# Kernel tuning notes

Measured on AMD Instinct MI355X. Metric: run time of the kernel, lower is better.

## Reference

```python
import jax, jax.numpy as jnp
import numpy as np

HEADS, HD = 8, 64

def swish(x):
    return x * jax.nn.sigmoid(x)

def layer_norm(x, eps=1e-5):
    mu = jnp.mean(x, axis=-1, keepdims=True)
    var = jnp.var(x, axis=-1, keepdims=True)
    return (x - mu) / jnp.sqrt(var + eps)

def setup_inputs() -> dict:
    key = jax.random.key(0)
    k1, k2, k3 = jax.random.split(key, 3)
    B, L, D = 2, 2048, 512
    x = jax.random.normal(k1, (B, L, D), jnp.float32)
    cnn_w = jax.random.normal(k2, (HEADS * HD * 3, D, 3), jnp.float32) * 0.02
    cnn_b = jnp.zeros((HEADS * HD * 3,), jnp.float32)
    fc_w = jax.random.normal(k3, (D, HEADS * HD), jnp.float32) * 0.02
    fc_b = jnp.zeros((D,), jnp.float32)
    return {"x": x, "cnn_w": cnn_w, "cnn_b": cnn_b, "fc_w": fc_w, "fc_b": fc_b}

def reference(x, cnn_w, cnn_b, fc_w, fc_b):
    B, L, D = x.shape
    # Conv1d(dims -> heads*hd*3, kernel=3, stride=1, pad=1) on channel-first layout
    xt = jnp.transpose(x, (0, 2, 1))  # [B, D, L]
    y = jax.lax.conv_general_dilated(
        xt, cnn_w, window_strides=(1,), padding=[(1, 1)],
        dimension_numbers=("NCH", "OIH", "NCH"),
    ) + cnn_b[None, :, None]  # [B, 3*H*HD, L]
    qkv = swish(y).reshape(B, HEADS, HD * 3, L)
    q, k, v = jnp.split(qkv, 3, axis=-2)  # each [B, H, HD, L]
    # NOTE: original scales by sqrt(length), not sqrt(hd)
    scores = jnp.einsum("bhdw,bhdm->bhwm", q, k) / jnp.sqrt(jnp.float32(L))
    att = jax.nn.softmax(scores, axis=-1)  # [B, H, L, L]
    new_v = jnp.einsum("bhwm,bhdm->bwhd", att, v).reshape(B, L, HEADS * HD)
    m = swish(new_v @ fc_w.T + fc_b)  # [B, L, D]
    return layer_norm(x * 2 + m)
```

## Files before the change

kernel.cpp:

```cpp
#include <hip/hip_runtime.h>
#include <hip/hip_bf16.h>

#define BB 2
#define LL 2048
#define DD 512
#define HH 8
#define HDM 64
#define SCALE 0.022097086912079608f
#define QSCALE 0.03187935766f

typedef __hip_bfloat16 bf16;
typedef unsigned short u16;
typedef __attribute__((ext_vector_type(8))) short short8v;
typedef __attribute__((ext_vector_type(4))) float float4v;

#define XN  2097152
#define WN  2359296
#define BN  1536
#define FWN 262144
#define FBN 512

__device__ __forceinline__ float b2f(u16 u) {
    return __uint_as_float(((unsigned int)u) << 16);
}
__device__ __forceinline__ u16 f2u(float f) {
    bf16 h = __float2bfloat16(f);
    u16 r;
    __builtin_memcpy(&r, &h, 2);
    return r;
}
__device__ __forceinline__ uint4 pack8(const float* f) {
    uint4 p;
    p.x = (unsigned)f2u(f[0]) | ((unsigned)f2u(f[1]) << 16);
    p.y = (unsigned)f2u(f[2]) | ((unsigned)f2u(f[3]) << 16);
    p.z = (unsigned)f2u(f[4]) | ((unsigned)f2u(f[5]) << 16);
    p.w = (unsigned)f2u(f[6]) | ((unsigned)f2u(f[7]) << 16);
    return p;
}

__device__ __forceinline__ void gld_lds16(const u16* g, u16* l) {
    __builtin_amdgcn_global_load_lds(
        (const __attribute__((address_space(1))) unsigned int*)g,
        (__attribute__((address_space(3))) unsigned int*)l, 16, 0, 0);
}

__device__ __forceinline__ int detect_flag(const u16* __restrict__ xraw) {
    int bad = 0;
    int lane = threadIdx.x & 63;
    for (int i = lane; i < 256; i += 64) {
        float v = b2f(xraw[i]);
        if (!(fabsf(v) < 100.f)) bad = 1;
    }
    return (__ballot(bad) != 0ull) ? 1 : 0;
}

__device__ __forceinline__ void conv8(const void* src, u16* dst, size_t i, int flag) {
    if (flag) {
        const float* s = (const float*)src;
        float f[8];
        float4 a = *(const float4*)(s + i);
        float4 b = *(const float4*)(s + i + 4);
        f[0] = a.x; f[1] = a.y; f[2] = a.z; f[3] = a.w;
        f[4] = b.x; f[5] = b.y; f[6] = b.z; f[7] = b.w;
        *(uint4*)(dst + i) = pack8(f);
    } else {
        *(uint4*)(dst + i) = *(const uint4*)((const u16*)src + i);
    }
}

__global__ __launch_bounds__(256) void prep_kernel(
    const void* __restrict__ xsrc, const void* __restrict__ wsrc,
    const void* __restrict__ bsrc, const void* __restrict__ fwsrc,
    const void* __restrict__ fbsrc,
    u16* __restrict__ xp, u16* __restrict__ wt,
    u16* __restrict__ bc, u16* __restrict__ fwc, u16* __restrict__ fbc)
{
    const int flag = detect_flag((const u16*)xsrc);
    const int bid = blockIdx.x;

    if (bid < 1024) {
        int idx = bid * 256 + threadIdx.x;
        if (idx < 256) {
            int b2  = idx >> 7;
            int r2  = (idx >> 6) & 1;
            int c82 = (idx & 63) * 8;
            size_t off = ((size_t)(b2 * 2050 + (r2 ? 2049 : 0))) * 512 + c82;
            uint4 z = {0u, 0u, 0u, 0u};
            *(uint4*)(xp + off) = z;
        }
        int b   = idx / (LL * 64);
        int rem = idx - b * (LL * 64);
        int l   = rem >> 6;
        int c8  = (rem & 63) * 8;
        size_t si = ((size_t)(b * LL + l)) * 512 + c8;
        size_t di = ((size_t)(b * 2050 + l + 1)) * 512 + c8;
        if (flag) {
            const float* s = (const float*)xsrc;
            float f[8];
            float4 a = *(const float4*)(s + si);
            float4 bq = *(const float4*)(s + si + 4);
            f[0] = a.x; f[1] = a.y; f[2] = a.z; f[3] = a.w;
            f[4] = bq.x; f[5] = bq.y; f[6] = bq.z; f[7] = bq.w;
            *(uint4*)(xp + di) = pack8(f);
        } else {
            *(uint4*)(xp + di) = *(const uint4*)((const u16*)xsrc + si);
        }
    } else if (bid < 2176) {
        int idx = (bid - 1024) * 256 + threadIdx.x;
        int i8  = idx & 63;
        int rem = idx >> 6;
        int k   = rem % 3;
        int o   = rem / 3;
        float f[8];
        if (flag) {
            const float* s = (const float*)wsrc;
#pragma unroll
            for (int j = 0; j < 8; ++j) f[j] = s[(size_t)o * 1536 + (i8 * 8 + j) * 3 + k];
        } else {
            const u16* s = (const u16*)wsrc;
#pragma unroll
            for (int j = 0; j < 8; ++j) f[j] = b2f(s[(size_t)o * 1536 + (i8 * 8 + j) * 3 + k]);
        }
        *(uint4*)(wt + (size_t)o * 1536 + k * 512 + i8 * 8) = pack8(f);
    } else {
        int o = (bid - 2176) * 256 + threadIdx.x;
        if (o < BN / 8) {
            conv8(bsrc, bc, (size_t)o * 8, flag);
        } else if (o < BN / 8 + FWN / 8) {
            conv8(fwsrc, fwc, (size_t)(o - BN / 8) * 8, flag);
        } else if (o < BN / 8 + FWN / 8 + FBN / 8) {
            conv8(fbsrc, fbc, (size_t)(o - BN / 8 - FWN / 8) * 8, flag);
        }
    }
}

__global__ __launch_bounds__(256) void conv_mfma_kernel(
    const u16* __restrict__ xp,
    const u16* __restrict__ wt,
    const u16* __restrict__ bias,
    u16* __restrict__ qkbuf,
    u16* __restrict__ vbuf)
{
    __shared__ u16 smem[32768];
    u16* Asb = smem;
    u16* Bsb = smem + 2 * 128 * 64;
#define OTS 140
    u16* OT  = smem;

    const int blk = blockIdx.x;
    const int rt = blk / 12;
    const int ct = blk - rt * 12;
    const int b  = rt >> 4;
    const int l0 = (rt & 15) * 128;
    const int tid  = threadIdx.x;
    const int wave = tid >> 6;
    const int lane = tid & 63;
    const int quad = lane >> 4;
    const int l16  = lane & 15;
    const int e7   = l16 & 7;
    const int wx = wave & 1;
    const int wy = wave >> 1;

    float4v acc[4][4];
#pragma unroll
    for (int mt = 0; mt < 4; ++mt)
#pragma unroll
        for (int nt = 0; nt < 4; ++nt) acc[mt][nt] = (float4v){0.f, 0.f, 0.f, 0.f};

    const int rowW = wave * 32;
    const int lrow = lane >> 3;
    const int g8   = (((lane & 7) ^ lrow)) * 8;
    auto stage = [&](int kc, int buf) {
        const int slab = kc >> 3;
        const int i0   = (kc & 7) * 64;
        const u16* ga = xp + ((size_t)(b * 2050 + l0 + rowW + slab + lrow)) * 512 + i0 + g8;
        const u16* gb = wt + ((size_t)(ct * 128 + rowW + lrow)) * 1536 + kc * 64 + g8;
        u16* la = Asb + (size_t)(buf * 128 + rowW) * 64;
        u16* lb = Bsb + (size_t)(buf * 128 + rowW) * 64;
#pragma unroll
        for (int j = 0; j < 4; ++j) {
            gld_lds16(ga + (size_t)(j * 8) * 512,  la + (j * 8) * 64);
            gld_lds16(gb + (size_t)(j * 8) * 1536, lb + (j * 8) * 64);
        }
    };

    stage(0, 0);

    for (int kc = 0; kc < 24; ++kc) {
        const int cur = kc & 1;
        __syncthreads();

        if (kc < 23) stage(kc + 1, 1 - cur);

#pragma unroll
        for (int half = 0; half < 2; ++half) {
            const int p = ((half * 4 + quad) ^ e7) * 8;
            short8v aF[4], bF[4];
#pragma unroll
            for (int mt = 0; mt < 4; ++mt)
                aF[mt] = *(const short8v*)&Asb[(size_t)(cur * 128 + wy * 64 + mt * 16 + l16) * 64 + p];
#pragma unroll
            for (int nt = 0; nt < 4; ++nt)
                bF[nt] = *(const short8v*)&Bsb[(size_t)(cur * 128 + wx * 64 + nt * 16 + l16) * 64 + p];
#pragma unroll
            for (int mt = 0; mt < 4; ++mt)
#pragma unroll
                for (int nt = 0; nt < 4; ++nt)
                    acc[mt][nt] = __builtin_amdgcn_mfma_f32_16x16x32_bf16(
                        aF[mt], bF[nt], acc[mt][nt], 0, 0, 0);
        }
    }

    __syncthreads();
    {
        const int tloc = (ct * 2 + wx) % 3;
#pragma unroll
        for (int nt = 0; nt < 4; ++nt) {
            int oc = wx * 64 + nt * 16 + l16;
            float bb = b2f(bias[ct * 128 + oc]);
#pragma unroll
            for (int mt = 0; mt < 4; ++mt)
#pragma unroll
                for (int r = 0; r < 4; ++r) {
                    int lr = wy * 64 + mt * 16 + quad * 4 + r;
                    float y = acc[mt][nt][r] + bb;
                    y = y / (1.f + __expf(-y));
                    if (tloc == 0) y *= QSCALE;
                    OT[lr * OTS + oc] = f2u(y);
                }
        }
    }
    __syncthreads();

#pragma unroll
    for (int g = 0; g < 2; ++g) {
        int a  = ct * 2 + g;
        int t  = a % 3;
        int bh = b * HH + a / 3;
        if (t != 2) {
            u16* base = qkbuf + ((size_t)((bh * 2 + t) * LL + l0)) * HDM;
#pragma unroll
            for (int it = 0; it < 4; ++it) {
                int idx = it * 256 + tid;
                int l   = idx >> 3;
                int d8  = (idx & 7) * 8;
                uint4 val = *(const uint4*)&OT[l * OTS + g * 64 + d8];
                *(uint4*)(base + (size_t)l * HDM + d8) = val;
            }
        } else {
            u16* base = vbuf + ((size_t)(bh * HDM)) * LL + l0;
#pragma unroll
            for (int it = 0; it < 4; ++it) {
                int idx = it * 256 + tid;
                int dd  = idx >> 4;
                int p   = idx & 15;
                int l8  = p * 8;
                u16 tmp[8];
#pragma unroll
                for (int j = 0; j < 8; ++j) tmp[j] = OT[(l8 + j) * OTS + g * 64 + dd];
                int a32 = p >> 2;
                int pb_ = p & 3;
                int q2  = (2 * pb_) & 3;
                int h2  = pb_ >> 1;
                int n0  = 32 * a32 + 8 * q2 + 4 * h2;
                uint2 v0, v1;
                v0.x = (unsigned)tmp[0] | ((unsigned)tmp[1] << 16);
                v0.y = (unsigned)tmp[2] | ((unsigned)tmp[3] << 16);
                v1.x = (unsigned)tmp[4] | ((unsigned)tmp[5] << 16);
                v1.y = (unsigned)tmp[6] | ((unsigned)tmp[7] << 16);
                *(uint2*)(base + (size_t)dd * LL + n0)     = v0;
                *(uint2*)(base + (size_t)dd * LL + n0 + 8) = v1;
            }
        }
    }
#undef OTS
}

__global__ __launch_bounds__(512) void attn_mfma_kernel(
    const u16* __restrict__ qk,
    const u16* __restrict__ v,
    u16* __restrict__ newv)
{
    __shared__ u16 smem[32768];
    u16 (*kts)[2][64][64] = (u16 (*)[2][64][64])smem;
    u16 (*vts)[2][64][64] = (u16 (*)[2][64][64])(smem + 16384);

    const int lb = ((blockIdx.x & 7) << 5) + (blockIdx.x >> 3);
    const int bh = lb >> 4;
    const int qc = lb & 15;
    const int b  = bh >> 3;
    const int h  = bh & 7;
    const int tid  = threadIdx.x;
    const int wave = tid >> 6;
    const int kg   = wave >> 2;
    const int qg   = wave & 3;
    const int lane = tid & 63;
    const int quad = lane >> 4;
    const int l16  = lane & 15;
    const int e7   = l16 & 7;

    const u16* qbase = qk + ((size_t)(bh * 2 + 0)) * LL * HDM;
    const u16* kbase = qk + ((size_t)(bh * 2 + 1)) * LL * HDM;
    const u16* vbase = v + (size_t)bh * HDM * LL;

    const int q0 = qc * 128 + qg * 32;

    short8v qfrag[2][2];
#pragma unroll
    for (int sg = 0; sg < 2; ++sg) {
        const u16* qr = qbase + (size_t)(q0 + sg * 16 + l16) * HDM + quad * 8;
        qfrag[sg][0] = *(const short8v*)(qr);
        qfrag[sg][1] = *(const short8v*)(qr + 32);
    }

    short8v vones;
    {
        short o1 = (l16 == 0) ? (short)0x3F80 : (short)0;
#pragma unroll
        for (int j = 0; j < 8; ++j) vones[j] = o1;
    }

    float4v oacc[2][4];
    float4v lacc[2];
#pragma unroll
    for (int sg = 0; sg < 2; ++sg) {
        lacc[sg] = (float4v){0.f, 0.f, 0.f, 0.f};
#pragma unroll
        for (int dt = 0; dt < 4; ++dt) oacc[sg][dt] = (float4v){0.f, 0.f, 0.f, 0.f};
    }

    const int rr  = qg * 8 + (lane >> 3);
    const int sw8 = ((lane & 7) ^ (lane >> 3)) * 8;
    auto stage = [&](int ic, int buf) {
        const int m0 = ic * 64;
#pragma unroll
        for (int r = 0; r < 2; ++r) {
            gld_lds16(kbase + (size_t)(m0 + r * 32 + rr) * HDM + sw8,
                      &kts[kg][buf][r * 32 + qg * 8][0]);
            gld_lds16(vbase + (size_t)(r * 32 + rr) * LL + m0 + sw8,
                      &vts[kg][buf][r * 32 + qg * 8][0]);
        }
    };

    stage(kg, 0);

    for (int i = 0; i < 16; ++i) {
        const int cur = i & 1;
        __syncthreads();

        if (i < 15) stage(2 * (i + 1) + kg, 1 - cur);

        float4v s[2][4];
#pragma unroll
        for (int mt = 0; mt < 4; ++mt) {
            short8v b0 = *(const short8v*)&kts[kg][cur][mt * 16 + l16][((quad) ^ e7) * 8];
            short8v b1 = *(const short8v*)&kts[kg][cur][mt * 16 + l16][((quad + 4) ^ e7) * 8];
#pragma unroll
            for (int sg = 0; sg < 2; ++sg) {
                float4v t = (float4v){0.f, 0.f, 0.f, 0.f};
                t = __builtin_amdgcn_mfma_f32_16x16x32_bf16(b0, qfrag[sg][0], t, 0, 0, 0);
                t = __builtin_amdgcn_mfma_f32_16x16x32_bf16(b1, qfrag[sg][1], t, 0, 0, 0);
                s[sg][mt] = t;
            }
        }

        unsigned pk[2][4][2];
#pragma unroll
        for (int sg = 0; sg < 2; ++sg)
#pragma unroll
            for (int mt = 0; mt < 4; ++mt) {
                float p0 = __builtin_amdgcn_exp2f(s[sg][mt][0]);
                float p1 = __builtin_amdgcn_exp2f(s[sg][mt][1]);
                float p2 = __builtin_amdgcn_exp2f(s[sg][mt][2]);
                float p3 = __builtin_amdgcn_exp2f(s[sg][mt][3]);
                pk[sg][mt][0] = (unsigned)f2u(p0) | ((unsigned)f2u(p1) << 16);
                pk[sg][mt][1] = (unsigned)f2u(p2) | ((unsigned)f2u(p3) << 16);
            }

#pragma unroll
        for (int mu = 0; mu < 2; ++mu) {
            short8v pb[2];
#pragma unroll
            for (int sg = 0; sg < 2; ++sg) {
                union { short8v v8; unsigned u[4]; } U;
                U.u[0] = pk[sg][2 * mu][0];
                U.u[1] = pk[sg][2 * mu][1];
                U.u[2] = pk[sg][2 * mu + 1][0];
                U.u[3] = pk[sg][2 * mu + 1][1];
                pb[sg] = U.v8;
                lacc[sg] = __builtin_amdgcn_mfma_f32_16x16x32_bf16(vones, pb[sg], lacc[sg], 0, 0, 0);
            }
#pragma unroll
            for (int dt = 0; dt < 4; ++dt) {
                short8v va = *(const short8v*)&vts[kg][cur][dt * 16 + l16][((mu * 4 + quad) ^ e7) * 8];
#pragma unroll
                for (int sg = 0; sg < 2; ++sg)
                    oacc[sg][dt] = __builtin_amdgcn_mfma_f32_16x16x32_bf16(va, pb[sg], oacc[sg][dt], 0, 0, 0);
            }
        }
    }

    float dnm[2];
#pragma unroll
    for (int sg = 0; sg < 2; ++sg) dnm[sg] = __shfl(lacc[sg][0], l16);

    __syncthreads();
    float* xch = (float*)smem;
    if (kg == 1) {
#pragma unroll
        for (int sg = 0; sg < 2; ++sg) {
#pragma unroll
            for (int dt = 0; dt < 4; ++dt)
#pragma unroll
                for (int r = 0; r < 4; ++r)
                    xch[((qg * 34 + (sg * 16 + dt * 4 + r)) << 6) + lane] = oacc[sg][dt][r];
            xch[((qg * 34 + 32 + sg) << 6) + lane] = dnm[sg];
        }
    }
    __syncthreads();
    if (kg == 0) {
        u16* ob = newv + (size_t)b * LL * 512 + h * 64;
#pragma unroll
        for (int sg = 0; sg < 2; ++sg) {
            float dt2 = dnm[sg] + xch[((qg * 34 + 32 + sg) << 6) + lane];
            float inv = 1.f / dt2;
            const size_t orow = (size_t)(q0 + sg * 16 + l16) * 512 + quad * 4;
#pragma unroll
            for (int dt = 0; dt < 4; ++dt) {
                float o0 = oacc[sg][dt][0] + xch[((qg * 34 + (sg * 16 + dt * 4 + 0)) << 6) + lane];
                float o1 = oacc[sg][dt][1] + xch[((qg * 34 + (sg * 16 + dt * 4 + 1)) << 6) + lane];
                float o2 = oacc[sg][dt][2] + xch[((qg * 34 + (sg * 16 + dt * 4 + 2)) << 6) + lane];
                float o3 = oacc[sg][dt][3] + xch[((qg * 34 + (sg * 16 + dt * 4 + 3)) << 6) + lane];
                unsigned lo = (unsigned)f2u(o0 * inv) | ((unsigned)f2u(o1 * inv) << 16);
                unsigned hi = (unsigned)f2u(o2 * inv) | ((unsigned)f2u(o3 * inv) << 16);
                uint2 val; val.x = lo; val.y = hi;
                *(uint2*)(ob + orow + dt * 16) = val;
            }
        }
    }
}

__global__ __launch_bounds__(256) void fc_ln_mfma_kernel(
    const u16* __restrict__ newv,
    const u16* __restrict__ fcw,
    const u16* __restrict__ fcb,
    const u16* __restrict__ xp,
    const u16* __restrict__ xraw,
    void* __restrict__ out)
{
    const int flag = detect_flag(xraw);
    const int l0 = blockIdx.x * 16;
    const int tid  = threadIdx.x;
    const int wave = tid >> 6;
    const int lane = tid & 63;
    const int quad = lane >> 4;
    const int l16  = lane & 15;
    const int col0 = wave * 128;

    const int bb_ = l0 >> 11;
    const size_t xbase = ((size_t)(bb_ * 2050 + (l0 & 2047) + 1)) * 512;

    __shared__ float psum[4][16], psq[4][16];

    short8v aF[16];
    const u16* arow = newv + (size_t)(l0 + l16) * 512 + quad * 8;
#pragma unroll
    for (int kc = 0; kc < 16; ++kc)
        aF[kc] = *(const short8v*)(arow + kc * 32);

    float4v acc[8];
#pragma unroll
    for (int nt = 0; nt < 8; ++nt) acc[nt] = (float4v){0.f, 0.f, 0.f, 0.f};

#pragma unroll
    for (int nt = 0; nt < 8; ++nt) {
        const u16* brow = fcw + (size_t)(col0 + nt * 16 + l16) * 512 + quad * 8;
#pragma unroll
        for (int kc = 0; kc < 16; ++kc) {
            short8v bF = *(const short8v*)(brow + kc * 32);
            acc[nt] = __builtin_amdgcn_mfma_f32_16x16x32_bf16(aF[kc], bF, acc[nt], 0, 0, 0);
        }
    }

    float z[8][4];
    float rs[4] = {0.f, 0.f, 0.f, 0.f}, rq[4] = {0.f, 0.f, 0.f, 0.f};
#pragma unroll
    for (int nt = 0; nt < 8; ++nt) {
        int col = col0 + nt * 16 + l16;
        float bb = b2f(fcb[col]);
#pragma unroll
        for (int r = 0; r < 4; ++r) {
            int row = quad * 4 + r;
            float y = acc[nt][r] + bb;
            float sw = y / (1.f + __expf(-y));
            float xv = b2f(xp[xbase + (size_t)row * 512 + col]);
            float zz = xv * 2.f + sw;
            z[nt][r] = zz;
            rs[r] += zz;
            rq[r] += zz * zz;
        }
    }
#pragma unroll
    for (int msk = 1; msk <= 8; msk <<= 1)
#pragma unroll
        for (int r = 0; r < 4; ++r) {
            rs[r] += __shfl_xor(rs[r], msk);
            rq[r] += __shfl_xor(rq[r], msk);
        }
    if (l16 == 0) {
#pragma unroll
        for (int r = 0; r < 4; ++r) {
            psum[wave][quad * 4 + r] = rs[r];
            psq[wave][quad * 4 + r]  = rq[r];
        }
    }
    __syncthreads();

    float mu[4], inv[4];
#pragma unroll
    for (int r = 0; r < 4; ++r) {
        int row = quad * 4 + r;
        float s = psum[0][row] + psum[1][row] + psum[2][row] + psum[3][row];
        float q = psq[0][row] + psq[1][row] + psq[2][row] + psq[3][row];
        float m = s * (1.f / 512.f);
        float var = q * (1.f / 512.f) - m * m;
        mu[r] = m;
        inv[r] = rsqrtf(var + 1e-5f);
    }

#pragma unroll
    for (int nt = 0; nt < 8; ++nt) {
        int col = col0 + nt * 16 + l16;
#pragma unroll
        for (int r = 0; r < 4; ++r) {
            int row = quad * 4 + r;
            float val = (z[nt][r] - mu[r]) * inv[r];
            if (flag) ((float*)out)[(size_t)(l0 + row) * 512 + col] = val;
            else      ((u16*)out)[(size_t)(l0 + row) * 512 + col] = f2u(val);
        }
    }
}

extern "C" void kernel_launch(void* const* d_in, const int* in_sizes, int n_in,
                              void* d_out, int out_size, void* d_ws, size_t ws_size,
                              hipStream_t stream) {
    (void)in_sizes; (void)n_in; (void)out_size; (void)ws_size;

    char* ws = (char*)d_ws;
    u16* xp   = (u16*)(ws + 256);
    u16* wtc  = (u16*)(ws + 4198656);
    u16* bc   = (u16*)(ws + 8917248);
    u16* fwc  = (u16*)(ws + 8920320);
    u16* fbc  = (u16*)(ws + 9444608);
    u16* qkb  = (u16*)(ws + 9445632);
    u16* vb   = (u16*)(ws + 17834240);
    u16* nvc  = (u16*)(ws + 22028544);

    prep_kernel<<<dim3(2305), dim3(256), 0, stream>>>(
        d_in[0], d_in[1], d_in[2], d_in[3], d_in[4],
        xp, wtc, bc, fwc, fbc);

    conv_mfma_kernel<<<dim3(32 * 12), dim3(256), 0, stream>>>(xp, wtc, bc, qkb, vb);
    attn_mfma_kernel<<<dim3(256), dim3(512), 0, stream>>>(qkb, vb, nvc);
    fc_ln_mfma_kernel<<<dim3(256), dim3(256), 0, stream>>>(
        nvc, fwc, fbc, xp, (const u16*)d_in[0], d_out);
}
```

Before: 154.9 us.

## Stage conv weight transpose through LDS and widen FC+LayerNorm block to 8 waves

The conv-weight repacking in the prep kernel now has each block load 8 output rows with coalesced vector loads into shared memory and do the (i,k)->(k,i) transpose there. Previously each thread made strided scalar global reads. The FC+LayerNorm kernel moves to 512 threads, each wave covering 64 output columns instead of 128. It stages the A tile in LDS via gld_lds16 with an XOR swizzle to cut redundant global loads and per-wave register pressure. The costs are extra LDS use, a barrier, and shared-memory reads with 3-element strides that can cause bank conflicts.

Result: faster. 149.1 us (-3.7%).

```diff
diff --git a/kernel.cpp b/kernel.cpp
--- a/kernel.cpp
+++ b/kernel.cpp
@@ -105,25 +105,49 @@
         } else {
             *(uint4*)(xp + di) = *(const uint4*)((const u16*)xsrc + si);
         }
-    } else if (bid < 2176) {
-        int idx = (bid - 1024) * 256 + threadIdx.x;
-        int i8  = idx & 63;
-        int rem = idx >> 6;
-        int k   = rem % 3;
-        int o   = rem / 3;
-        float f[8];
+    } else if (bid < 1216) {
+        __shared__ u16 wl[8 * 1536];
+        const int t  = threadIdx.x;
+        const int o0 = (bid - 1024) * 8;
         if (flag) {
-            const float* s = (const float*)wsrc;
-#pragma unroll
-            for (int j = 0; j < 8; ++j) f[j] = s[(size_t)o * 1536 + (i8 * 8 + j) * 3 + k];
+            const float4* s4 = (const float4*)((const float*)wsrc + (size_t)o0 * 1536);
+#pragma unroll
+            for (int v = 0; v < 12; ++v) {
+                int i4 = v * 256 + t;
+                float4 q = s4[i4];
+                uint2 p;
+                p.x = (unsigned)f2u(q.x) | ((unsigned)f2u(q.y) << 16);
+                p.y = (unsigned)f2u(q.z) | ((unsigned)f2u(q.w) << 16);
+                *(uint2*)&wl[i4 * 4] = p;
+            }
         } else {
-            const u16* s = (const u16*)wsrc;
-#pragma unroll
-            for (int j = 0; j < 8; ++j) f[j] = b2f(s[(size_t)o * 1536 + (i8 * 8 + j) * 3 + k]);
-        }
-        *(uint4*)(wt + (size_t)o * 1536 + k * 512 + i8 * 8) = pack8(f);
+            const uint4* s8 = (const uint4*)((const u16*)wsrc + (size_t)o0 * 1536);
+#pragma unroll
+            for (int v = 0; v < 6; ++v) {
+                int i8 = v * 256 + t;
+                *(uint4*)&wl[i8 * 8] = s8[i8];
+            }
+        }
+        __syncthreads();
+#pragma unroll
+        for (int v = 0; v < 6; ++v) {
+            int oct = v * 256 + t;
+            int row = oct / 192;
+            int rem = oct - row * 192;
+            int k   = rem >> 6;
+            int i8  = rem & 63;
+            u16 tmp[8];
+#pragma unroll
+            for (int j = 0; j < 8; ++j) tmp[j] = wl[row * 1536 + (i8 * 8 + j) * 3 + k];
+            uint4 val;
+            val.x = (unsigned)tmp[0] | ((unsigned)tmp[1] << 16);
+            val.y = (unsigned)tmp[2] | ((unsigned)tmp[3] << 16);
+            val.z = (unsigned)tmp[4] | ((unsigned)tmp[5] << 16);
+            val.w = (unsigned)tmp[6] | ((unsigned)tmp[7] << 16);
+            *(uint4*)(wt + (size_t)(o0 + row) * 1536 + k * 512 + i8 * 8) = val;
+        }
     } else {
-        int o = (bid - 2176) * 256 + threadIdx.x;
+        int o = (bid - 1216) * 256 + threadIdx.x;
         if (o < BN / 8) {
             conv8(bsrc, bc, (size_t)o * 8, flag);
         } else if (o < BN / 8 + FWN / 8) {
@@ -440,7 +464,7 @@
     }
 }
 
-__global__ __launch_bounds__(256) void fc_ln_mfma_kernel(
+__global__ __launch_bounds__(512) void fc_ln_mfma_kernel(
     const u16* __restrict__ newv,
     const u16* __restrict__ fcw,
     const u16* __restrict__ fcb,
@@ -455,25 +479,33 @@
     const int lane = tid & 63;
     const int quad = lane >> 4;
     const int l16  = lane & 15;
-    const int col0 = wave * 128;
+    const int col0 = wave * 64;
 
     const int bb_ = l0 >> 11;
     const size_t xbase = ((size_t)(bb_ * 2050 + (l0 & 2047) + 1)) * 512;
 
-    __shared__ float psum[4][16], psq[4][16];
+    __shared__ u16 As[16][512];
+    __shared__ float psum[8][16], psq[8][16];
+
+#pragma unroll
+    for (int r = 0; r < 2; ++r) {
+        const int row = wave + r * 8;
+        gld_lds16(newv + (size_t)(l0 + row) * 512 + ((lane ^ (row & 7)) * 8),
+                  &As[row][0]);
+    }
+    __syncthreads();
 
     short8v aF[16];
-    const u16* arow = newv + (size_t)(l0 + l16) * 512 + quad * 8;
 #pragma unroll
     for (int kc = 0; kc < 16; ++kc)
-        aF[kc] = *(const short8v*)(arow + kc * 32);
-
-    float4v acc[8];
-#pragma unroll
-    for (int nt = 0; nt < 8; ++nt) acc[nt] = (float4v){0.f, 0.f, 0.f, 0.f};
-
-#pragma unroll
-    for (int nt = 0; nt < 8; ++nt) {
+        aF[kc] = *(const short8v*)&As[l16][(((kc * 4 + quad)) ^ (l16 & 7)) * 8];
+
+    float4v acc[4];
+#pragma unroll
+    for (int nt = 0; nt < 4; ++nt) acc[nt] = (float4v){0.f, 0.f, 0.f, 0.f};
+
+#pragma unroll
+    for (int nt = 0; nt < 4; ++nt) {
         const u16* brow = fcw + (size_t)(col0 + nt * 16 + l16) * 512 + quad * 8;
 #pragma unroll
         for (int kc = 0; kc < 16; ++kc) {
@@ -482,10 +514,10 @@
         }
     }
 
-    float z[8][4];
+    float z[4][4];
     float rs[4] = {0.f, 0.f, 0.f, 0.f}, rq[4] = {0.f, 0.f, 0.f, 0.f};
 #pragma unroll
-    for (int nt = 0; nt < 8; ++nt) {
+    for (int nt = 0; nt < 4; ++nt) {
         int col = col0 + nt * 16 + l16;
         float bb = b2f(fcb[col]);
 #pragma unroll
@@ -520,8 +552,9 @@
 #pragma unroll
     for (int r = 0; r < 4; ++r) {
         int row = quad * 4 + r;
-        float s = psum[0][row] + psum[1][row] + psum[2][row] + psum[3][row];
-        float q = psq[0][row] + psq[1][row] + psq[2][row] + psq[3][row];
+        float s = 0.f, q = 0.f;
+#pragma unroll
+        for (int w = 0; w < 8; ++w) { s += psum[w][row]; q += psq[w][row]; }
         float m = s * (1.f / 512.f);
         float var = q * (1.f / 512.f) - m * m;
         mu[r] = m;
@@ -529,7 +562,7 @@
     }
 
 #pragma unroll
-    for (int nt = 0; nt < 8; ++nt) {
+    for (int nt = 0; nt < 4; ++nt) {
         int col = col0 + nt * 16 + l16;
 #pragma unroll
         for (int r = 0; r < 4; ++r) {
@@ -556,12 +589,12 @@
     u16* vb   = (u16*)(ws + 17834240);
     u16* nvc  = (u16*)(ws + 22028544);
 
-    prep_kernel<<<dim3(2305), dim3(256), 0, stream>>>(
+    prep_kernel<<<dim3(1345), dim3(256), 0, stream>>>(
         d_in[0], d_in[1], d_in[2], d_in[3], d_in[4],
         xp, wtc, bc, fwc, fbc);
 
     conv_mfma_kernel<<<dim3(32 * 12), dim3(256), 0, stream>>>(xp, wtc, bc, qkb, vb);
     attn_mfma_kernel<<<dim3(256), dim3(512), 0, stream>>>(qkb, vb, nvc);
-    fc_ln_mfma_kernel<<<dim3(256), dim3(256), 0, stream>>>(
+    fc_ln_mfma_kernel<<<dim3(256), dim3(512), 0, stream>>>(
         nvc, fwc, fbc, xp, (const u16*)d_in[0], d_out);
 }
```
